# Optimization experiments

Measured on AMD Instinct MI355X. Metric: run time of the kernel, lower is better.

The kernel has to match this reference:

```python
import jax, jax.numpy as jnp
import numpy as np

B, D, L, E, R = 16384, 2048, 3, 8, 64


def setup_inputs() -> dict:
    key = jax.random.key(0)
    k1, k2, k3, k4 = jax.random.split(key, 4)
    scale = 1.0 / np.sqrt(D)  # ~ PyTorch Linear default init scale
    X0 = jax.random.normal(k1, (B, D), dtype=jnp.float32)
    U = jax.random.normal(k2, (L, E, R, D), dtype=jnp.float32) * scale
    V = jax.random.normal(k3, (L, E, R, D), dtype=jnp.float32) * scale
    Wg = jax.random.normal(k4, (L, E, D), dtype=jnp.float32) * scale
    bg = jnp.zeros((L, E), dtype=jnp.float32)
    return {"X0": X0, "U": U, "V": V, "Wg": Wg, "bg": bg}


def reference(X0, U, V, Wg, bg):
    # X0: (B, D); U, V: (L, E, R, D); Wg: (L, E, D); bg: (L, E)
    Xi = X0
    num_layers = U.shape[0]
    for l in range(num_layers):  # small fixed layer count
        gate = jax.nn.softmax(jnp.einsum('bd,ed->be', Xi, Wg[l]) + bg[l], axis=1)  # (B, E)
        Uo = jnp.einsum('bd,erd->ber', Xi, U[l])  # (B, E, R)
        Vo = jnp.einsum('bd,erd->ber', Xi, V[l])  # (B, E, R)
        expert_out = jnp.sum(Uo * Vo, axis=2)     # (B, E) low-rank bilinear forms
        xw = jnp.sum(expert_out * gate, axis=1, keepdims=True)  # (B, 1)
        Xi = Xi + X0 * xw  # residual cross update (dropout=0, eval mode)
    return Xi
```

## Files before the change

kernel.cpp:

```cpp
#include <hip/hip_runtime.h>
#include <hip/hip_bf16.h>

#define BDIM 16384
#define DDIM 2048
#define LNUM 3
#define ENUM 8
#define NP 24
#define NPG 25

#define BM 256
#define BK 32

typedef _Float16 f16x8 __attribute__((ext_vector_type(8)));
typedef _Float16 f16x4 __attribute__((ext_vector_type(4)));
typedef float f32x4 __attribute__((ext_vector_type(4)));

__global__ void cvt_w_kernel(const float* __restrict__ U, const float* __restrict__ V,
                             _Float16* __restrict__ Wh) {
    size_t f = (size_t)blockIdx.x * blockDim.x + threadIdx.x;
    size_t elem = f * 4;
    int d   = (int)(elem & (DDIM - 1));
    int row = (int)((elem >> 11) & 127);
    int p   = (int)(elem >> 18);
    const float* src = (row < 64)
        ? (U + ((size_t)(p * 64 + row) * DDIM + d))
        : (V + ((size_t)(p * 64 + (row - 64)) * DDIM + d));
    float4 v = *(const float4*)src;
    f16x4 h = { (_Float16)v.x, (_Float16)v.y, (_Float16)v.z, (_Float16)v.w };
    ((f16x4*)Wh)[f] = h;
}

__global__ void cvt_wg_kernel(const float* __restrict__ Wg, _Float16* __restrict__ Wgh) {
    int f = (int)(blockIdx.x * blockDim.x + threadIdx.x);
    float4 v = ((const float4*)Wg)[f];
    f16x4 h = { (_Float16)v.x, (_Float16)v.y, (_Float16)v.z, (_Float16)v.w };
    ((f16x4*)Wgh)[f] = h;
}

__global__ void cvt_x_kernel(const float* __restrict__ X0, _Float16* __restrict__ X0h) {
    size_t f = (size_t)blockIdx.x * blockDim.x + threadIdx.x;
    float4 v = ((const float4*)X0)[f];
    f16x4 h = { (_Float16)v.x, (_Float16)v.y, (_Float16)v.z, (_Float16)v.w };
    ((f16x4*)X0h)[f] = h;
}

__global__ __launch_bounds__(256, 2) void gemm_t_kernel(
    const _Float16* __restrict__ Ah,
    const _Float16* __restrict__ Bh,
    const _Float16* __restrict__ Wgh,
    float* __restrict__ T,
    float* __restrict__ G)
{
    const int p    = blockIdx.y;
    const int m0   = blockIdx.x * BM;
    const int tid  = (int)threadIdx.x;
    const int wave = tid >> 6;
    const int lane = tid & 63;
    const int mlane = lane & 15;
    const int quad  = lane >> 4;

    __shared__ _Float16 As[BM * BK];
    __shared__ _Float16 Bs[128 * BK];

    f32x4 acc[4][8];
#pragma unroll
    for (int i = 0; i < 4; ++i)
#pragma unroll
        for (int j = 0; j < 8; ++j) acc[i][j] = (f32x4){0.f, 0.f, 0.f, 0.f};

    const int srow = lane >> 2;
    const int scol = ((lane & 3) ^ ((lane >> 3) & 3)) * 8;
    const int sw   = (mlane >> 1) & 3;

    const bool gate = (p == NP);
    const _Float16* Bp = gate ? Wgh : (Bh + (size_t)p * 128 * DDIM);

    for (int k0 = 0; k0 < DDIM; k0 += BK) {
        __syncthreads();
#pragma unroll
        for (int q = 0; q < 4; ++q) {
            int r16 = wave * 64 + q * 16;
            const _Float16* ga = Ah + (size_t)(m0 + r16 + srow) * DDIM + k0 + scol;
            __builtin_amdgcn_global_load_lds(
                (const __attribute__((address_space(1))) void*)ga,
                (__attribute__((address_space(3))) void*)&As[r16 * BK], 16, 0, 0);
        }
#pragma unroll
        for (int q = 0; q < 2; ++q) {
            int r16 = wave * 32 + q * 16;
            int r   = r16 + srow;
            int rb  = (gate && r >= NP) ? (r & 15) : r;
            const _Float16* gb = Bp + (size_t)rb * DDIM + k0 + scol;
            __builtin_amdgcn_global_load_lds(
                (const __attribute__((address_space(1))) void*)gb,
                (__attribute__((address_space(3))) void*)&Bs[r16 * BK], 16, 0, 0);
        }
        __syncthreads();

        f16x8 aF[4], bF[8];
#pragma unroll
        for (int mi = 0; mi < 4; ++mi)
            aF[mi] = *(const f16x8*)&As[(wave * 64 + mi * 16 + mlane) * BK + ((quad ^ sw) * 8)];
#pragma unroll
        for (int ni = 0; ni < 8; ++ni)
            bF[ni] = *(const f16x8*)&Bs[(ni * 16 + mlane) * BK + ((quad ^ sw) * 8)];
#pragma unroll
        for (int mi = 0; mi < 4; ++mi)
#pragma unroll
            for (int ni = 0; ni < 8; ++ni)
                acc[mi][ni] = __builtin_amdgcn_mfma_f32_16x16x32_f16(
                    aF[mi], bF[ni], acc[mi][ni], 0, 0, 0);
    }

    if (!gate) {
#pragma unroll
        for (int mi = 0; mi < 4; ++mi) {
#pragma unroll
            for (int j = 0; j < 4; ++j) {
                float tp = 0.f;
#pragma unroll
                for (int ni = 0; ni < 4; ++ni)
                    tp += acc[mi][ni][j] * acc[mi][ni + 4][j];
                tp += __shfl_xor(tp, 1);
                tp += __shfl_xor(tp, 2);
                tp += __shfl_xor(tp, 4);
                tp += __shfl_xor(tp, 8);
                if (mlane == 0) {
                    int m = wave * 64 + mi * 16 + quad * 4 + j;
                    T[(size_t)p * BDIM + (m0 + m)] = tp;
                }
            }
        }
    } else {
#pragma unroll
        for (int mi = 0; mi < 4; ++mi)
#pragma unroll
            for (int ni = 0; ni < 2; ++ni) {
                int col = ni * 16 + mlane;
                if (col < NP) {
#pragma unroll
                    for (int j = 0; j < 4; ++j) {
                        int m = wave * 64 + mi * 16 + quad * 4 + j;
                        G[(size_t)col * BDIM + (m0 + m)] = acc[mi][ni][j];
                    }
                }
            }
    }
}

__global__ void epilogue_kernel(const _Float16* __restrict__ X0h,
                                const float* __restrict__ T,
                                const float* __restrict__ G,
                                const float* __restrict__ bg,
                                float* __restrict__ out) {
    __shared__ float s_sh[16];
    const int b0 = blockIdx.x * 16;
    const int tid = (int)threadIdx.x;
    if (tid < 16) {
        int b = b0 + tid;
        float s = 1.f;
#pragma unroll
        for (int l = 0; l < LNUM; ++l) {
            float logit[ENUM];
            float mx = -1e30f;
#pragma unroll
            for (int e = 0; e < ENUM; ++e) {
                int j = l * ENUM + e;
                float g = s * G[(size_t)j * BDIM + b] + bg[j];
                logit[e] = g;
                mx = fmaxf(mx, g);
            }
            float den = 0.f, num = 0.f;
            float s2 = s * s;
#pragma unroll
            for (int e = 0; e < ENUM; ++e) {
                int j = l * ENUM + e;
                float w = __expf(logit[e] - mx);
                den += w;
                num += w * (s2 * T[(size_t)j * BDIM + b]);
            }
            s += num / den;
        }
        s_sh[tid] = s;
    }
    __syncthreads();
    const int nf4 = DDIM / 4;
    for (int idx = tid; idx < 16 * nf4; idx += 256) {
        int r = idx >> 9;
        int c = idx & (nf4 - 1);
        float s = s_sh[r];
        f16x4 h = ((const f16x4*)(X0h + (size_t)(b0 + r) * DDIM))[c];
        float4 x = { s * (float)h[0], s * (float)h[1], s * (float)h[2], s * (float)h[3] };
        ((float4*)(out + (size_t)(b0 + r) * DDIM))[c] = x;
    }
}

extern "C" void kernel_launch(void* const* d_in, const int* in_sizes, int n_in,
                              void* d_out, int out_size, void* d_ws, size_t ws_size,
                              hipStream_t stream) {
    const float* X0 = (const float*)d_in[0];
    const float* U  = (const float*)d_in[1];
    const float* V  = (const float*)d_in[2];
    const float* Wg = (const float*)d_in[3];
    const float* bg = (const float*)d_in[4];
    float* out = (float*)d_out;

    char* ws = (char*)d_ws;
    _Float16* X0h = (_Float16*)ws;
    _Float16* Wh  = (_Float16*)(ws + 67108864ull);
    _Float16* Wgh = (_Float16*)(ws + 79691776ull);
    float* T      = (float*)(ws + 79790080ull);
    float* G      = (float*)(ws + 81362944ull);

    cvt_w_kernel<<<dim3((NP * 128 * DDIM / 4) / 256), dim3(256), 0, stream>>>(U, V, Wh);
    cvt_wg_kernel<<<dim3((NP * DDIM / 4) / 256), dim3(256), 0, stream>>>(Wg, Wgh);
    cvt_x_kernel<<<dim3((BDIM * DDIM / 4) / 256), dim3(256), 0, stream>>>(X0, X0h);
    gemm_t_kernel<<<dim3(BDIM / BM, NPG), dim3(256), 0, stream>>>(X0h, Wh, Wgh, T, G);
    epilogue_kernel<<<dim3(BDIM / 16), dim3(256), 0, stream>>>(X0h, T, G, bg, out);
}
```

Baseline: 524.1 us.

## Double-buffer GEMM with BK=64 and 512-thread blocks covering two projections

Restructures the fp16 MFMA GEMM to use 512-thread blocks, where each block computes two U/V projection groups (256 output columns) against a 256-row A tile. The gate GEMM gets a block of its own. K-tiles of 64 are double-buffered in LDS through async global_load_lds with explicit vmcnt waits, so loads overlap compute, and s_setprio is raised around the MFMA sections. Each A tile is now reused across twice as many columns, halving A reloads. The gate block wastes half its compute on duplicated rows. LDS use per block rises to 128 KB, which may limit occupancy.

```diff
diff --git a/kernel.cpp b/kernel.cpp
--- a/kernel.cpp
+++ b/kernel.cpp
@@ -6,10 +6,10 @@
 #define LNUM 3
 #define ENUM 8
 #define NP 24
-#define NPG 25
 
 #define BM 256
-#define BK 32
+#define BK 64
+#define NT (DDIM / BK)
 
 typedef _Float16 f16x8 __attribute__((ext_vector_type(8)));
 typedef _Float16 f16x4 __attribute__((ext_vector_type(4)));
@@ -44,23 +44,48 @@
     ((f16x4*)X0h)[f] = h;
 }
 
-__global__ __launch_bounds__(256, 2) void gemm_t_kernel(
+__global__ __launch_bounds__(512, 2) void gemm_t_kernel(
     const _Float16* __restrict__ Ah,
     const _Float16* __restrict__ Bh,
     const _Float16* __restrict__ Wgh,
     float* __restrict__ T,
     float* __restrict__ G)
 {
-    const int p    = blockIdx.y;
+    const int by   = blockIdx.y;
     const int m0   = blockIdx.x * BM;
     const int tid  = (int)threadIdx.x;
     const int wave = tid >> 6;
     const int lane = tid & 63;
+    const int wm   = wave >> 1;
+    const int wc   = wave & 1;
     const int mlane = lane & 15;
     const int quad  = lane >> 4;
-
-    __shared__ _Float16 As[BM * BK];
-    __shared__ _Float16 Bs[128 * BK];
+    const bool gateblk = (by == 12);
+
+    __shared__ _Float16 Ls[2][2][BM * BK];
+
+    const _Float16* aptr[4];
+    const _Float16* bptr[4];
+#pragma unroll
+    for (int q = 0; q < 4; ++q) {
+        int idx = q * 512 + tid;
+        int row = idx >> 3;
+        int c   = idx & 7;
+        int col = ((c ^ (row & 7)) * 8);
+        aptr[q] = Ah + (size_t)(m0 + row) * DDIM + col;
+        int s = row >> 7;
+        int brow = row & 127;
+        const _Float16* base;
+        int br;
+        if (gateblk) {
+            base = Wgh;
+            br = (s == 0 && brow < NP) ? brow : (brow & 15);
+        } else {
+            base = Bh + (size_t)(2 * by + s) * 128 * DDIM;
+            br = brow;
+        }
+        bptr[q] = base + (size_t)br * DDIM + col;
+    }
 
     f32x4 acc[4][8];
 #pragma unroll
@@ -68,51 +93,89 @@
 #pragma unroll
         for (int j = 0; j < 8; ++j) acc[i][j] = (f32x4){0.f, 0.f, 0.f, 0.f};
 
-    const int srow = lane >> 2;
-    const int scol = ((lane & 3) ^ ((lane >> 3) & 3)) * 8;
-    const int sw   = (mlane >> 1) & 3;
-
-    const bool gate = (p == NP);
-    const _Float16* Bp = gate ? Wgh : (Bh + (size_t)p * 128 * DDIM);
-
-    for (int k0 = 0; k0 < DDIM; k0 += BK) {
-        __syncthreads();
-#pragma unroll
-        for (int q = 0; q < 4; ++q) {
-            int r16 = wave * 64 + q * 16;
-            const _Float16* ga = Ah + (size_t)(m0 + r16 + srow) * DDIM + k0 + scol;
+#pragma unroll
+    for (int tt = 0; tt < 2; ++tt) {
+#pragma unroll
+        for (int q = 0; q < 4; ++q)
             __builtin_amdgcn_global_load_lds(
-                (const __attribute__((address_space(1))) void*)ga,
-                (__attribute__((address_space(3))) void*)&As[r16 * BK], 16, 0, 0);
-        }
-#pragma unroll
-        for (int q = 0; q < 2; ++q) {
-            int r16 = wave * 32 + q * 16;
-            int r   = r16 + srow;
-            int rb  = (gate && r >= NP) ? (r & 15) : r;
-            const _Float16* gb = Bp + (size_t)rb * DDIM + k0 + scol;
+                (const __attribute__((address_space(1))) void*)(aptr[q] + tt * BK),
+                (__attribute__((address_space(3))) void*)&Ls[tt][0][(q * 512 + wave * 64) * 8],
+                16, 0, 0);
+#pragma unroll
+        for (int q = 0; q < 4; ++q)
             __builtin_amdgcn_global_load_lds(
-                (const __attribute__((address_space(1))) void*)gb,
-                (__attribute__((address_space(3))) void*)&Bs[r16 * BK], 16, 0, 0);
-        }
-        __syncthreads();
-
-        f16x8 aF[4], bF[8];
+                (const __attribute__((address_space(1))) void*)(bptr[q] + tt * BK),
+                (__attribute__((address_space(3))) void*)&Ls[tt][1][(q * 512 + wave * 64) * 8],
+                16, 0, 0);
+    }
+
+    int cur = 0;
+    for (int t = 0; t < NT; ++t) {
+        if (t < NT - 1) asm volatile("s_waitcnt vmcnt(8)" ::: "memory");
+        else            asm volatile("s_waitcnt vmcnt(0)" ::: "memory");
+        __builtin_amdgcn_s_barrier();
+
+        const _Float16* Asc = &Ls[cur][0][0];
+        const _Float16* Bsc = &Ls[cur][1][0];
+#pragma unroll
+        for (int ks = 0; ks < 2; ++ks) {
+            f16x8 aF[4], bF[8];
+#pragma unroll
+            for (int mi = 0; mi < 4; ++mi) {
+                int row = wm * 64 + mi * 16 + mlane;
+                aF[mi] = *(const f16x8*)&Asc[row * BK + (((ks * 4 + quad) ^ (row & 7)) * 8)];
+            }
+#pragma unroll
+            for (int ni = 0; ni < 8; ++ni) {
+                int row = wc * 128 + ni * 16 + mlane;
+                bF[ni] = *(const f16x8*)&Bsc[row * BK + (((ks * 4 + quad) ^ (row & 7)) * 8)];
+            }
+            __builtin_amdgcn_s_setprio(1);
+#pragma unroll
+            for (int mi = 0; mi < 4; ++mi)
+#pragma unroll
+                for (int ni = 0; ni < 8; ++ni)
+                    acc[mi][ni] = __builtin_amdgcn_mfma_f32_16x16x32_f16(
+                        aF[mi], bF[ni], acc[mi][ni], 0, 0, 0);
+            __builtin_amdgcn_s_setprio(0);
+        }
+
+        __builtin_amdgcn_s_barrier();
+        if (t + 2 < NT) {
+            int k0 = (t + 2) * BK;
+#pragma unroll
+            for (int q = 0; q < 4; ++q)
+                __builtin_amdgcn_global_load_lds(
+                    (const __attribute__((address_space(1))) void*)(aptr[q] + k0),
+                    (__attribute__((address_space(3))) void*)&Ls[cur][0][(q * 512 + wave * 64) * 8],
+                    16, 0, 0);
+#pragma unroll
+            for (int q = 0; q < 4; ++q)
+                __builtin_amdgcn_global_load_lds(
+                    (const __attribute__((address_space(1))) void*)(bptr[q] + k0),
+                    (__attribute__((address_space(3))) void*)&Ls[cur][1][(q * 512 + wave * 64) * 8],
+                    16, 0, 0);
+        }
+        cur ^= 1;
+    }
+
+    if (gateblk) {
+        if (wc == 1) return;
 #pragma unroll
         for (int mi = 0; mi < 4; ++mi)
-            aF[mi] = *(const f16x8*)&As[(wave * 64 + mi * 16 + mlane) * BK + ((quad ^ sw) * 8)];
-#pragma unroll
-        for (int ni = 0; ni < 8; ++ni)
-            bF[ni] = *(const f16x8*)&Bs[(ni * 16 + mlane) * BK + ((quad ^ sw) * 8)];
-#pragma unroll
-        for (int mi = 0; mi < 4; ++mi)
-#pragma unroll
-            for (int ni = 0; ni < 8; ++ni)
-                acc[mi][ni] = __builtin_amdgcn_mfma_f32_16x16x32_f16(
-                    aF[mi], bF[ni], acc[mi][ni], 0, 0, 0);
-    }
-
-    if (!gate) {
+#pragma unroll
+            for (int ni = 0; ni < 2; ++ni) {
+                int col = ni * 16 + mlane;
+                if (col < NP) {
+#pragma unroll
+                    for (int j = 0; j < 4; ++j) {
+                        int m = wm * 64 + mi * 16 + quad * 4 + j;
+                        G[(size_t)col * BDIM + (m0 + m)] = acc[mi][ni][j];
+                    }
+                }
+            }
+    } else {
+        const int p = 2 * by + wc;
 #pragma unroll
         for (int mi = 0; mi < 4; ++mi) {
 #pragma unroll
@@ -126,25 +189,11 @@
                 tp += __shfl_xor(tp, 4);
                 tp += __shfl_xor(tp, 8);
                 if (mlane == 0) {
-                    int m = wave * 64 + mi * 16 + quad * 4 + j;
+                    int m = wm * 64 + mi * 16 + quad * 4 + j;
                     T[(size_t)p * BDIM + (m0 + m)] = tp;
                 }
             }
         }
-    } else {
-#pragma unroll
-        for (int mi = 0; mi < 4; ++mi)
-#pragma unroll
-            for (int ni = 0; ni < 2; ++ni) {
-                int col = ni * 16 + mlane;
-                if (col < NP) {
-#pragma unroll
-                    for (int j = 0; j < 4; ++j) {
-                        int m = wave * 64 + mi * 16 + quad * 4 + j;
-                        G[(size_t)col * BDIM + (m0 + m)] = acc[mi][ni][j];
-                    }
-                }
-            }
     }
 }
 
@@ -215,6 +264,6 @@
     cvt_w_kernel<<<dim3((NP * 128 * DDIM / 4) / 256), dim3(256), 0, stream>>>(U, V, Wh);
     cvt_wg_kernel<<<dim3((NP * DDIM / 4) / 256), dim3(256), 0, stream>>>(Wg, Wgh);
     cvt_x_kernel<<<dim3((BDIM * DDIM / 4) / 256), dim3(256), 0, stream>>>(X0, X0h);
-    gemm_t_kernel<<<dim3(BDIM / BM, NPG), dim3(256), 0, stream>>>(X0h, Wh, Wgh, T, G);
+    gemm_t_kernel<<<dim3(BDIM / BM, 13), dim3(512), 0, stream>>>(X0h, Wh, Wgh, T, G);
     epilogue_kernel<<<dim3(BDIM / 16), dim3(256), 0, stream>>>(X0h, T, G, bg, out);
 }
```

Measured after the change: 492.2 us. 1.06x faster.
